# Optimization experiments

Measured on AMD Instinct MI355X. Metric: run time of the kernel, lower is better.

The kernel has to match this reference:

```python
import jax, jax.numpy as jnp
import numpy as np

N_NODES = 100_000
N_EDGES = 1_600_000
N_FEAT = 64
HIDDEN = 64
BIOPRINT = 2048
N_GRAPHS = 1024


def setup_inputs() -> dict:
    key = jax.random.key(0)
    ks = jax.random.split(key, 12)
    x = jax.random.normal(ks[0], (N_NODES, N_FEAT), jnp.float32)
    edge_index = jax.random.randint(ks[1], (2, N_EDGES), 0, N_NODES, dtype=jnp.int64)
    batch = jnp.sort(jax.random.randint(ks[2], (N_NODES,), 0, N_GRAPHS, dtype=jnp.int64))
    def lin(k, fan_in, fan_out):
        s = 1.0 / np.sqrt(fan_in)
        return jax.random.uniform(k, (fan_in, fan_out), jnp.float32, -s, s)
    W1 = lin(ks[3], N_FEAT, HIDDEN)
    b1 = jnp.zeros((HIDDEN,), jnp.float32)
    W2 = lin(ks[4], HIDDEN, HIDDEN)
    b2 = jnp.zeros((HIDDEN,), jnp.float32)
    W3 = lin(ks[5], HIDDEN, HIDDEN)
    b3 = jnp.zeros((HIDDEN,), jnp.float32)
    Wd = lin(ks[6], HIDDEN, BIOPRINT)
    bd = jax.random.uniform(ks[7], (BIOPRINT,), jnp.float32, -1.0 / np.sqrt(HIDDEN), 1.0 / np.sqrt(HIDDEN))
    return {"x": x, "edge_index": edge_index, "batch": batch,
            "W1": W1, "b1": b1, "W2": W2, "b2": b2, "W3": W3, "b3": b3,
            "Wd": Wd, "bd": bd}


def reference(x, edge_index, batch, W1, b1, W2, b2, W3, b3, Wd, bd):
    n = x.shape[0]
    src, dst = edge_index[0], edge_index[1]
    # GCN symmetric normalization with self-loops: deg = in-degree + 1
    ones_e = jnp.ones(src.shape[0], x.dtype)
    deg = jax.ops.segment_sum(ones_e, dst, num_segments=n) + 1.0
    dinv = jax.lax.rsqrt(deg)  # deg >= 1 always
    self_norm = (dinv * dinv)[:, None]
    edge_norm = (dinv[src] * dinv[dst])[:, None]

    def gcn_conv(h, W, b):
        hw = h @ W  # [N, out]
        agg = jax.ops.segment_sum(hw[src] * edge_norm, dst, num_segments=n)
        return agg + hw * self_norm + b  # self-loop handled analytically

    h = jax.nn.relu(gcn_conv(x, W1, b1))
    h = jax.nn.relu(gcn_conv(h, W2, b2))
    h = gcn_conv(h, W3, b3)

    # global_mean_pool over graph ids
    cnt = jax.ops.segment_sum(jnp.ones(n, x.dtype), batch, num_segments=N_GRAPHS)
    pooled = jax.ops.segment_sum(h, batch, num_segments=N_GRAPHS) / jnp.maximum(cnt, 1.0)[:, None]

    # dropout(p=0.5) is identity in eval mode
    logits = pooled @ Wd + bd
    probs = jax.nn.softmax(logits, axis=-1)
    return (probs >= 0.5).astype(x.dtype)
```

## Files before the change

kernel.cpp:

```cpp
#include <hip/hip_runtime.h>
#include <hip/hip_fp16.h>
#include <math.h>

#define N_NODES   100000
#define N_EDGES   1600000
#define N_FEAT    64
#define HIDDEN    64
#define BIOPRINT  2048
#define N_GRAPHS  1024

#define SENTINEL  N_NODES
#define ELL_STRIDE 64

#define N_E4 (N_EDGES / 4)
#define FILL_BLOCKS ((N_E4 + 255) / 256)
#define MM1_BLOCKS (N_NODES / 32)
#define GS_BLOCKS  5

#define XCD_SLICE 12500
#define CHUNK_SHIFT 15
#define CH4 (1 << (CHUNK_SHIFT - 2))
#define NC 49
#define SLOT_P 56
#define CNT_BLOCKS (8 * SLOT_P)
#define PREP_BLOCKS ((N_NODES + 255) / 256)

__device__ __forceinline__ __half2 shx_h2(__half2 v, int m) {
    int x = __shfl_xor(*(int*)&v, m);
    return *(__half2*)&x;
}

__device__ __forceinline__ void stage_w_perm(const float* __restrict__ W, float* sW, int t) {
    const float4* W4 = (const float4*)W;
    for (int i = t; i < 1024; i += 256) {
        float4 w = W4[i];
        int k = i >> 4;
        int c4 = (i & 15) * 4;
        int base = (k >> 2) * 256 + (k & 3);
        sW[base + (c4 + 0) * 4] = w.x;
        sW[base + (c4 + 1) * 4] = w.y;
        sW[base + (c4 + 2) * 4] = w.z;
        sW[base + (c4 + 3) * 4] = w.w;
    }
}

__global__ __launch_bounds__(256) void k_count(
        const int* __restrict__ dst, int* __restrict__ counts,
        int* __restrict__ rankl) {
    int p = blockIdx.x / SLOT_P;
    int c = blockIdx.x % SLOT_P;
    if (c >= NC) return;
    __shared__ int hist[XCD_SLICE];
    int t = threadIdx.x;
    for (int i = t; i < XCD_SLICE; i += 256) hist[i] = 0;
    __syncthreads();
    int lo = p * XCD_SLICE, hi = lo + XCD_SLICE;
    int base4 = c * CH4;
    int end4 = base4 + CH4; if (end4 > N_E4) end4 = N_E4;
    const int4* dst4 = (const int4*)dst;
    for (int i4 = base4 + t; i4 < end4; i4 += 256) {
        int4 d4 = dst4[i4];
        int e = i4 * 4;
        if (d4.x >= lo && d4.x < hi) rankl[e + 0] = atomicAdd(&hist[d4.x - lo], 1);
        if (d4.y >= lo && d4.y < hi) rankl[e + 1] = atomicAdd(&hist[d4.y - lo], 1);
        if (d4.z >= lo && d4.z < hi) rankl[e + 2] = atomicAdd(&hist[d4.z - lo], 1);
        if (d4.w >= lo && d4.w < hi) rankl[e + 3] = atomicAdd(&hist[d4.w - lo], 1);
    }
    __syncthreads();
    int* crow = counts + (size_t)c * N_NODES + lo;
    for (int i = t; i < XCD_SLICE; i += 256) crow[i] = hist[i];
}

__global__ __launch_bounds__(256) void k_prep(
        int* __restrict__ counts, int* __restrict__ deg, float* __restrict__ dinv,
        const int* __restrict__ batch, int* __restrict__ gstart) {
    int bid = blockIdx.x, t = threadIdx.x;
    if (bid < PREP_BLOCKS) {
        int n = bid * 256 + t;
        if (n >= N_NODES) return;
        int s = 0;
#pragma unroll
        for (int c = 0; c < NC; ++c) {
            size_t idx = (size_t)c * N_NODES + n;
            int v = counts[idx];
            counts[idx] = s;
            s += v;
        }
        deg[n] = s;
        dinv[n] = rsqrtf((float)s + 1.0f);
        return;
    }
    int g = (bid - PREP_BLOCKS) * 256 + t;
    if (g > N_GRAPHS) return;
    if (g == N_GRAPHS) { gstart[g] = N_NODES; return; }
    int lo = 0, hi = N_NODES;
    while (lo < hi) { int mid = (lo + hi) >> 1; if (batch[mid] < g) lo = mid + 1; else hi = mid; }
    gstart[g] = lo;
}

__global__ __launch_bounds__(256) void k_fillmm(
        const int* __restrict__ src, const int* __restrict__ dst,
        const int* __restrict__ rankl, const int* __restrict__ counts,
        int* __restrict__ colELL,
        const int* __restrict__ deg, const float* __restrict__ dinv,
        const float* __restrict__ x, const float* __restrict__ W,
        __half* __restrict__ hw) {
    int bid = blockIdx.x, t = threadIdx.x;
    if (bid < FILL_BLOCKS) {
        int tid = bid * 256 + t;
        if (tid < N_E4) {
            int e = tid * 4;
            const int* pref = counts + (size_t)(e >> CHUNK_SHIFT) * N_NODES;
            int4 d4 = ((const int4*)dst)[tid];
            int4 r4 = ((const int4*)rankl)[tid];
            int4 s4 = ((const int4*)src)[tid];
            int px = pref[d4.x] + r4.x; colELL[d4.x * ELL_STRIDE + (px & 63)] = s4.x;
            int py = pref[d4.y] + r4.y; colELL[d4.y * ELL_STRIDE + (py & 63)] = s4.y;
            int pz = pref[d4.z] + r4.z; colELL[d4.z * ELL_STRIDE + (pz & 63)] = s4.z;
            int pw = pref[d4.w] + r4.w; colELL[d4.w * ELL_STRIDE + (pw & 63)] = s4.w;
        }
        return;
    }
    bid -= FILL_BLOCKS;
    __shared__ float sW[64 * 64];
    __shared__ float sA[32 * 64];
    stage_w_perm(W, sW, t);
    int row0 = bid * 32;
    ((float4*)sA)[t]       = ((const float4*)x)[row0 * 16 + t];
    ((float4*)sA)[t + 256] = ((const float4*)x)[row0 * 16 + t + 256];
    __syncthreads();
    int wave = t >> 6, lane = t & 63;
    const float4* sWp = (const float4*)sW;
    float sum[8] = {0.f, 0.f, 0.f, 0.f, 0.f, 0.f, 0.f, 0.f};
#pragma unroll
    for (int k4 = 0; k4 < 16; ++k4) {
        float4 w4 = sWp[k4 * 64 + lane];
#pragma unroll
        for (int hh = 0; hh < 8; ++hh) {
            float4 a4 = ((const float4*)&sA[(wave * 8 + hh) * 64])[k4];
            sum[hh] = fmaf(a4.x, w4.x, sum[hh]);
            sum[hh] = fmaf(a4.y, w4.y, sum[hh]);
            sum[hh] = fmaf(a4.z, w4.z, sum[hh]);
            sum[hh] = fmaf(a4.w, w4.w, sum[hh]);
        }
    }
#pragma unroll
    for (int hh = 0; hh < 8; ++hh) {
        int row = row0 + wave * 8 + hh;
        hw[(size_t)row * 64 + lane] = __float2half_rn(sum[hh] * dinv[row]);
    }
    if (t < 32) {
        int r2 = row0 + t;
        int dv = deg[r2]; if (dv > 64) dv = 64;
        int vp = (dv + 15) & ~15;
        for (int j = dv; j < vp; ++j) colELL[r2 * ELL_STRIDE + j] = SENTINEL;
    }
}

__device__ __forceinline__ void gather2x8(
        const int* __restrict__ col, const uint4* __restrict__ hv,
        int rs, int re, int slot, int sub, float f[8]) {
    __half2 a0 = __float2half2_rn(0.f), a1 = a0, a2 = a0, a3 = a0;
    __half2 c0 = a0, c1 = a0, c2 = a0, c3 = a0;
    for (int e = rs; e < re; e += 16) {
        int s0 = __builtin_nontemporal_load(&col[e + slot]);
        int s1 = __builtin_nontemporal_load(&col[e + 2 + slot]);
        int s2 = __builtin_nontemporal_load(&col[e + 4 + slot]);
        int s3 = __builtin_nontemporal_load(&col[e + 6 + slot]);
        int s4 = __builtin_nontemporal_load(&col[e + 8 + slot]);
        int s5 = __builtin_nontemporal_load(&col[e + 10 + slot]);
        int s6 = __builtin_nontemporal_load(&col[e + 12 + slot]);
        int s7 = __builtin_nontemporal_load(&col[e + 14 + slot]);
        uint4 u0 = hv[(size_t)s0 * 8 + sub];
        uint4 u1 = hv[(size_t)s1 * 8 + sub];
        uint4 u2 = hv[(size_t)s2 * 8 + sub];
        uint4 u3 = hv[(size_t)s3 * 8 + sub];
        uint4 u4 = hv[(size_t)s4 * 8 + sub];
        uint4 u5 = hv[(size_t)s5 * 8 + sub];
        uint4 u6 = hv[(size_t)s6 * 8 + sub];
        uint4 u7 = hv[(size_t)s7 * 8 + sub];
        a0 = __hadd2(a0, *(__half2*)&u0.x); a1 = __hadd2(a1, *(__half2*)&u0.y);
        a2 = __hadd2(a2, *(__half2*)&u0.z); a3 = __hadd2(a3, *(__half2*)&u0.w);
        c0 = __hadd2(c0, *(__half2*)&u1.x); c1 = __hadd2(c1, *(__half2*)&u1.y);
        c2 = __hadd2(c2, *(__half2*)&u1.z); c3 = __hadd2(c3, *(__half2*)&u1.w);
        a0 = __hadd2(a0, *(__half2*)&u2.x); a1 = __hadd2(a1, *(__half2*)&u2.y);
        a2 = __hadd2(a2, *(__half2*)&u2.z); a3 = __hadd2(a3, *(__half2*)&u2.w);
        c0 = __hadd2(c0, *(__half2*)&u3.x); c1 = __hadd2(c1, *(__half2*)&u3.y);
        c2 = __hadd2(c2, *(__half2*)&u3.z); c3 = __hadd2(c3, *(__half2*)&u3.w);
        a0 = __hadd2(a0, *(__half2*)&u4.x); a1 = __hadd2(a1, *(__half2*)&u4.y);
        a2 = __hadd2(a2, *(__half2*)&u4.z); a3 = __hadd2(a3, *(__half2*)&u4.w);
        c0 = __hadd2(c0, *(__half2*)&u5.x); c1 = __hadd2(c1, *(__half2*)&u5.y);
        c2 = __hadd2(c2, *(__half2*)&u5.z); c3 = __hadd2(c3, *(__half2*)&u5.w);
        a0 = __hadd2(a0, *(__half2*)&u6.x); a1 = __hadd2(a1, *(__half2*)&u6.y);
        a2 = __hadd2(a2, *(__half2*)&u6.z); a3 = __hadd2(a3, *(__half2*)&u6.w);
        c0 = __hadd2(c0, *(__half2*)&u7.x); c1 = __hadd2(c1, *(__half2*)&u7.y);
        c2 = __hadd2(c2, *(__half2*)&u7.z); c3 = __hadd2(c3, *(__half2*)&u7.w);
    }
    a0 = __hadd2(a0, c0); a1 = __hadd2(a1, c1);
    a2 = __hadd2(a2, c2); a3 = __hadd2(a3, c3);
    a0 = __hadd2(a0, shx_h2(a0, 8));
    a1 = __hadd2(a1, shx_h2(a1, 8));
    a2 = __hadd2(a2, shx_h2(a2, 8));
    a3 = __hadd2(a3, shx_h2(a3, 8));
    float2 f0 = __half22float2(a0), f1 = __half22float2(a1);
    float2 f2 = __half22float2(a2), f3 = __half22float2(a3);
    f[0] = f0.x; f[1] = f0.y; f[2] = f1.x; f[3] = f1.y;
    f[4] = f2.x; f[5] = f2.y; f[6] = f3.x; f[7] = f3.y;
}

__global__ __launch_bounds__(256) void k_gmm(
        const int* __restrict__ deg, const int* __restrict__ col,
        const float* __restrict__ dinv, const float* __restrict__ b,
        const __half* __restrict__ hw_in, const float* __restrict__ W,
        __half* __restrict__ hw_out) {
    __shared__ float sW[64 * 64];
    __shared__ float sA[16 * 64];
    int t = threadIdx.x;
    stage_w_perm(W, sW, t);
    __syncthreads();

    int wave = t >> 6, lane = t & 63;
    int quarter = lane >> 4, slot = (lane >> 3) & 1, sub = lane & 7;
    int i0 = blockIdx.x * 16 + wave * 4;
    int i = i0 + quarter;
    float di = dinv[i];
    int dv = deg[i]; if (dv > 64) dv = 64;
    int rs = i * ELL_STRIDE;
    int re = rs + ((dv + 15) & ~15);
    const uint4* hv = (const uint4*)hw_in;

    float f[8];
    gather2x8(col, hv, rs, re, slot, sub, f);

    uint4 us = hv[(size_t)i * 8 + sub];
    float2 s0 = __half22float2(*(__half2*)&us.x);
    float2 s1 = __half22float2(*(__half2*)&us.y);
    float2 s2 = __half22float2(*(__half2*)&us.z);
    float2 s3 = __half22float2(*(__half2*)&us.w);
    float sf[8] = {s0.x, s0.y, s1.x, s1.y, s2.x, s2.y, s3.x, s3.y};
    float4 ba = ((const float4*)b)[sub * 2];
    float4 bb = ((const float4*)b)[sub * 2 + 1];
    float bf[8] = {ba.x, ba.y, ba.z, ba.w, bb.x, bb.y, bb.z, bb.w};
    if (slot == 0) {
        float r[8];
#pragma unroll
        for (int k = 0; k < 8; ++k) r[k] = fmaxf(fmaf(di, f[k] + sf[k], bf[k]), 0.f);
        *(float4*)&sA[(wave * 4 + quarter) * 64 + sub * 8]     = make_float4(r[0], r[1], r[2], r[3]);
        *(float4*)&sA[(wave * 4 + quarter) * 64 + sub * 8 + 4] = make_float4(r[4], r[5], r[6], r[7]);
    }

    const float4* sWp = (const float4*)sW;
    float sum[4] = {0.f, 0.f, 0.f, 0.f};
#pragma unroll
    for (int k4 = 0; k4 < 16; ++k4) {
        float4 w4 = sWp[k4 * 64 + lane];
#pragma unroll
        for (int hh = 0; hh < 4; ++hh) {
            float4 a4 = ((const float4*)&sA[(wave * 4 + hh) * 64])[k4];
            sum[hh] = fmaf(a4.x, w4.x, sum[hh]);
            sum[hh] = fmaf(a4.y, w4.y, sum[hh]);
            sum[hh] = fmaf(a4.z, w4.z, sum[hh]);
            sum[hh] = fmaf(a4.w, w4.w, sum[hh]);
        }
    }
#pragma unroll
    for (int hh = 0; hh < 4; ++hh)
        hw_out[(size_t)(i0 + hh) * 64 + lane] = __float2half_rn(sum[hh] * dinv[i0 + hh]);
}

__global__ __launch_bounds__(256) void k_gather3(
        const int* __restrict__ deg, const int* __restrict__ col,
        const float* __restrict__ dinv, const float* __restrict__ b,
        const __half* __restrict__ hw_in, __half* __restrict__ conv) {
    int t = threadIdx.x;
    int wave = t >> 6, lane = t & 63;
    int quarter = lane >> 4, slot = (lane >> 3) & 1, sub = lane & 7;
    int i = blockIdx.x * 16 + wave * 4 + quarter;
    float di = dinv[i];
    int dv = deg[i]; if (dv > 64) dv = 64;
    int rs = i * ELL_STRIDE;
    int re = rs + ((dv + 15) & ~15);
    const uint4* hv = (const uint4*)hw_in;

    float f[8];
    gather2x8(col, hv, rs, re, slot, sub, f);

    if (slot == 0) {
        uint4 us = hv[(size_t)i * 8 + sub];
        float2 s0 = __half22float2(*(__half2*)&us.x);
        float2 s1 = __half22float2(*(__half2*)&us.y);
        float2 s2 = __half22float2(*(__half2*)&us.z);
        float2 s3 = __half22float2(*(__half2*)&us.w);
        float sf[8] = {s0.x, s0.y, s1.x, s1.y, s2.x, s2.y, s3.x, s3.y};
        float4 ba = ((const float4*)b)[sub * 2];
        float4 bb = ((const float4*)b)[sub * 2 + 1];
        float bf[8] = {ba.x, ba.y, ba.z, ba.w, bb.x, bb.y, bb.z, bb.w};
        uint4 o;
        __half2* oh = (__half2*)&o;
#pragma unroll
        for (int c = 0; c < 4; ++c) {
            float r0 = fmaf(di, f[2 * c] + sf[2 * c], bf[2 * c]);
            float r1 = fmaf(di, f[2 * c + 1] + sf[2 * c + 1], bf[2 * c + 1]);
            oh[c] = __halves2half2(__float2half_rn(r0), __float2half_rn(r1));
        }
        ((uint4*)conv)[(size_t)i * 8 + sub] = o;
    }
}

__global__ __launch_bounds__(256) void k_dense(
        const __half* __restrict__ conv, const int* __restrict__ gstart,
        const float* __restrict__ Wd, const float* __restrict__ bd,
        float* __restrict__ out) {
    __shared__ float sred[4][64];
    __shared__ float sp[64];
    __shared__ float rmax[4];
    __shared__ float rsum[4];
    int t = threadIdx.x;
    int wave = t >> 6, lane = t & 63;
    int g = blockIdx.x;
    int n0 = gstart[g], n1 = gstart[g + 1];

    int fp = lane & 31;
    int par = lane >> 5;
    const __half2* conv2 = (const __half2*)conv;
    float2 acc2 = make_float2(0.f, 0.f);
    for (int i = n0 + wave * 2 + par; i < n1; i += 8) {
        float2 f = __half22float2(conv2[(size_t)i * 32 + fp]);
        acc2.x += f.x; acc2.y += f.y;
    }
    acc2.x += __shfl_xor(acc2.x, 32);
    acc2.y += __shfl_xor(acc2.y, 32);
    if (lane < 32) { sred[wave][2 * fp] = acc2.x; sred[wave][2 * fp + 1] = acc2.y; }
    __syncthreads();
    if (t < 64) {
        int n = n1 - n0;
        float s = sred[0][t] + sred[1][t] + sred[2][t] + sred[3][t];
        sp[t] = (n > 0) ? s / (float)n : 0.f;
    }
    __syncthreads();

    float acc[8];
#pragma unroll
    for (int r = 0; r < 8; ++r) acc[r] = bd[r * 256 + t];
    for (int k = 0; k < 64; ++k) {
        float h = sp[k];
#pragma unroll
        for (int r = 0; r < 8; ++r)
            acc[r] = fmaf(h, Wd[k * BIOPRINT + r * 256 + t], acc[r]);
    }

    float m = acc[0];
#pragma unroll
    for (int r = 1; r < 8; ++r) m = fmaxf(m, acc[r]);
#pragma unroll
    for (int off = 32; off > 0; off >>= 1) m = fmaxf(m, __shfl_xor(m, off));
    if (lane == 0) rmax[wave] = m;
    __syncthreads();
    m = fmaxf(fmaxf(rmax[0], rmax[1]), fmaxf(rmax[2], rmax[3]));

    float s = 0.f;
#pragma unroll
    for (int r = 0; r < 8; ++r) { acc[r] = expf(acc[r] - m); s += acc[r]; }
#pragma unroll
    for (int off = 32; off > 0; off >>= 1) s += __shfl_xor(s, off);
    if (lane == 0) rsum[wave] = s;
    __syncthreads();
    s = rsum[0] + rsum[1] + rsum[2] + rsum[3];

#pragma unroll
    for (int r = 0; r < 8; ++r) {
        float p = acc[r] / s;
        out[(size_t)g * BIOPRINT + r * 256 + t] = (p >= 0.5f) ? 1.0f : 0.0f;
    }
}


extern "C" void kernel_launch(void* const* d_in, const int* in_sizes, int n_in,
                              void* d_out, int out_size, void* d_ws, size_t ws_size,
                              hipStream_t stream) {
    const float* x     = (const float*)d_in[0];
    const int*   ei    = (const int*)d_in[1];
    const int*   batch = (const int*)d_in[2];
    const float* W1 = (const float*)d_in[3];
    const float* b1 = (const float*)d_in[4];
    const float* W2 = (const float*)d_in[5];
    const float* b2 = (const float*)d_in[6];
    const float* W3 = (const float*)d_in[7];
    const float* b3 = (const float*)d_in[8];
    const float* Wd = (const float*)d_in[9];
    const float* bd = (const float*)d_in[10];
    float* out = (float*)d_out;

    const int* src = ei;
    const int* dst = ei + N_EDGES;

    char* ws = (char*)d_ws;
    size_t off = 0;
    auto alloc = [&](size_t bytes) {
        void* p = ws + off;
        off += (bytes + 255) & ~(size_t)255;
        return p;
    };
    int*    deg    = (int*)alloc(N_NODES * sizeof(int));
    float*  dinv   = (float*)alloc(N_NODES * sizeof(float));
    int*    rank   = (int*)alloc((size_t)N_EDGES * sizeof(int));
    int*    gstart = (int*)alloc((N_GRAPHS + 1) * sizeof(int));
    int*    counts = (int*)alloc((size_t)NC * N_NODES * sizeof(int));
    int*    colELL = (int*)alloc((size_t)N_NODES * ELL_STRIDE * sizeof(int));
    __half* bufA   = (__half*)alloc((size_t)(N_NODES + 1) * HIDDEN * sizeof(__half));
    __half* bufB   = (__half*)alloc((size_t)(N_NODES + 1) * HIDDEN * sizeof(__half));
    __half* conv   = (__half*)alloc((size_t)N_NODES * HIDDEN * sizeof(__half));

    hipMemsetAsync(bufA + (size_t)N_NODES * HIDDEN, 0, HIDDEN * sizeof(__half), stream);
    hipMemsetAsync(bufB + (size_t)N_NODES * HIDDEN, 0, HIDDEN * sizeof(__half), stream);

    k_count<<<CNT_BLOCKS, 256, 0, stream>>>(dst, counts, rank);
    k_prep<<<PREP_BLOCKS + GS_BLOCKS, 256, 0, stream>>>(counts, deg, dinv, batch, gstart);
    k_fillmm<<<FILL_BLOCKS + MM1_BLOCKS, 256, 0, stream>>>(
        src, dst, rank, counts, colELL, deg, dinv, x, W1, bufA);

    const int g16_grid = N_NODES / 16;
    k_gmm<<<g16_grid, 256, 0, stream>>>(deg, colELL, dinv, b1, bufA, W2, bufB);
    k_gmm<<<g16_grid, 256, 0, stream>>>(deg, colELL, dinv, b2, bufB, W3, bufA);
    k_gather3<<<g16_grid, 256, 0, stream>>>(deg, colELL, dinv, b3, bufA, conv);
    k_dense<<<N_GRAPHS, 256, 0, stream>>>(conv, gstart, Wd, bd, out);
}
```

Before: 316.4 us.

## Shrink count/rank arrays and move first matmul into count kernel

The per-chunk prefix counts are stored as 16-bit and the per-edge local ranks as 8-bit, which cuts the traffic of the count, prep and fill stages. The layer-1 x@W1 matmul moves into the count kernel, where it runs alongside the histogram blocks. The dinv scaling is now applied in a separate in-place pass inside the fill kernel. In exchange the fill kernel does an extra read-modify-write of bufA, and the 8-bit ranks assume per-chunk, per-node counts stay below 256.

Measured after the change: 309.2 us. 2.3% less time.

```diff
diff --git a/kernel.cpp b/kernel.cpp
--- a/kernel.cpp
+++ b/kernel.cpp
@@ -24,6 +24,9 @@
 #define SLOT_P 56
 #define CNT_BLOCKS (8 * SLOT_P)
 #define PREP_BLOCKS ((N_NODES + 255) / 256)
+
+typedef unsigned short u16;
+typedef unsigned char  u8;
 
 __device__ __forceinline__ __half2 shx_h2(__half2 v, int m) {
     int x = __shfl_xor(*(int*)&v, m);
@@ -44,35 +47,68 @@
     }
 }
 
-__global__ __launch_bounds__(256) void k_count(
-        const int* __restrict__ dst, int* __restrict__ counts,
-        int* __restrict__ rankl) {
-    int p = blockIdx.x / SLOT_P;
-    int c = blockIdx.x % SLOT_P;
-    if (c >= NC) return;
-    __shared__ int hist[XCD_SLICE];
-    int t = threadIdx.x;
-    for (int i = t; i < XCD_SLICE; i += 256) hist[i] = 0;
-    __syncthreads();
-    int lo = p * XCD_SLICE, hi = lo + XCD_SLICE;
-    int base4 = c * CH4;
-    int end4 = base4 + CH4; if (end4 > N_E4) end4 = N_E4;
-    const int4* dst4 = (const int4*)dst;
-    for (int i4 = base4 + t; i4 < end4; i4 += 256) {
-        int4 d4 = dst4[i4];
-        int e = i4 * 4;
-        if (d4.x >= lo && d4.x < hi) rankl[e + 0] = atomicAdd(&hist[d4.x - lo], 1);
-        if (d4.y >= lo && d4.y < hi) rankl[e + 1] = atomicAdd(&hist[d4.y - lo], 1);
-        if (d4.z >= lo && d4.z < hi) rankl[e + 2] = atomicAdd(&hist[d4.z - lo], 1);
-        if (d4.w >= lo && d4.w < hi) rankl[e + 3] = atomicAdd(&hist[d4.w - lo], 1);
-    }
-    __syncthreads();
-    int* crow = counts + (size_t)c * N_NODES + lo;
-    for (int i = t; i < XCD_SLICE; i += 256) crow[i] = hist[i];
+__global__ __launch_bounds__(256) void k_countmm(
+        const int* __restrict__ dst, u16* __restrict__ counts, u8* __restrict__ rankl,
+        const float* __restrict__ x, const float* __restrict__ W,
+        __half* __restrict__ hw) {
+    __shared__ int smem[XCD_SLICE];
+    int bid = blockIdx.x, t = threadIdx.x;
+    if (bid < CNT_BLOCKS) {
+        int p = bid / SLOT_P;
+        int c = bid % SLOT_P;
+        if (c >= NC) return;
+        int* hist = smem;
+        for (int i = t; i < XCD_SLICE; i += 256) hist[i] = 0;
+        __syncthreads();
+        int lo = p * XCD_SLICE, hi = lo + XCD_SLICE;
+        int base4 = c * CH4;
+        int end4 = base4 + CH4; if (end4 > N_E4) end4 = N_E4;
+        const int4* dst4 = (const int4*)dst;
+        for (int i4 = base4 + t; i4 < end4; i4 += 256) {
+            int4 d4 = dst4[i4];
+            int e = i4 * 4;
+            if (d4.x >= lo && d4.x < hi) rankl[e + 0] = (u8)atomicAdd(&hist[d4.x - lo], 1);
+            if (d4.y >= lo && d4.y < hi) rankl[e + 1] = (u8)atomicAdd(&hist[d4.y - lo], 1);
+            if (d4.z >= lo && d4.z < hi) rankl[e + 2] = (u8)atomicAdd(&hist[d4.z - lo], 1);
+            if (d4.w >= lo && d4.w < hi) rankl[e + 3] = (u8)atomicAdd(&hist[d4.w - lo], 1);
+        }
+        __syncthreads();
+        u16* crow = counts + (size_t)c * N_NODES + lo;
+        for (int i = t; i < XCD_SLICE; i += 256) crow[i] = (u16)hist[i];
+        return;
+    }
+    bid -= CNT_BLOCKS;
+    float* sW = (float*)smem;
+    float* sA = (float*)smem + 4096;
+    stage_w_perm(W, sW, t);
+    int row0 = bid * 32;
+    ((float4*)sA)[t]       = ((const float4*)x)[row0 * 16 + t];
+    ((float4*)sA)[t + 256] = ((const float4*)x)[row0 * 16 + t + 256];
+    __syncthreads();
+    int wave = t >> 6, lane = t & 63;
+    const float4* sWp = (const float4*)sW;
+    float sum[8] = {0.f, 0.f, 0.f, 0.f, 0.f, 0.f, 0.f, 0.f};
+#pragma unroll
+    for (int k4 = 0; k4 < 16; ++k4) {
+        float4 w4 = sWp[k4 * 64 + lane];
+#pragma unroll
+        for (int hh = 0; hh < 8; ++hh) {
+            float4 a4 = ((const float4*)&sA[(wave * 8 + hh) * 64])[k4];
+            sum[hh] = fmaf(a4.x, w4.x, sum[hh]);
+            sum[hh] = fmaf(a4.y, w4.y, sum[hh]);
+            sum[hh] = fmaf(a4.z, w4.z, sum[hh]);
+            sum[hh] = fmaf(a4.w, w4.w, sum[hh]);
+        }
+    }
+#pragma unroll
+    for (int hh = 0; hh < 8; ++hh) {
+        int row = row0 + wave * 8 + hh;
+        hw[(size_t)row * 64 + lane] = __float2half_rn(sum[hh]);
+    }
 }
 
 __global__ __launch_bounds__(256) void k_prep(
-        int* __restrict__ counts, int* __restrict__ deg, float* __restrict__ dinv,
+        u16* __restrict__ counts, int* __restrict__ deg, float* __restrict__ dinv,
         const int* __restrict__ batch, int* __restrict__ gstart) {
     int bid = blockIdx.x, t = threadIdx.x;
     if (bid < PREP_BLOCKS) {
@@ -83,7 +119,7 @@
         for (int c = 0; c < NC; ++c) {
             size_t idx = (size_t)c * N_NODES + n;
             int v = counts[idx];
-            counts[idx] = s;
+            counts[idx] = (u16)s;
             s += v;
         }
         deg[n] = s;
@@ -98,21 +134,20 @@
     gstart[g] = lo;
 }
 
-__global__ __launch_bounds__(256) void k_fillmm(
+__global__ __launch_bounds__(256) void k_fillscale(
         const int* __restrict__ src, const int* __restrict__ dst,
-        const int* __restrict__ rankl, const int* __restrict__ counts,
+        const u8* __restrict__ rankl, const u16* __restrict__ counts,
         int* __restrict__ colELL,
         const int* __restrict__ deg, const float* __restrict__ dinv,
-        const float* __restrict__ x, const float* __restrict__ W,
         __half* __restrict__ hw) {
     int bid = blockIdx.x, t = threadIdx.x;
     if (bid < FILL_BLOCKS) {
         int tid = bid * 256 + t;
         if (tid < N_E4) {
             int e = tid * 4;
-            const int* pref = counts + (size_t)(e >> CHUNK_SHIFT) * N_NODES;
+            const u16* pref = counts + (size_t)(e >> CHUNK_SHIFT) * N_NODES;
             int4 d4 = ((const int4*)dst)[tid];
-            int4 r4 = ((const int4*)rankl)[tid];
+            uchar4 r4 = ((const uchar4*)rankl)[tid];
             int4 s4 = ((const int4*)src)[tid];
             int px = pref[d4.x] + r4.x; colELL[d4.x * ELL_STRIDE + (px & 63)] = s4.x;
             int py = pref[d4.y] + r4.y; colELL[d4.y * ELL_STRIDE + (py & 63)] = s4.y;
@@ -122,33 +157,18 @@
         return;
     }
     bid -= FILL_BLOCKS;
-    __shared__ float sW[64 * 64];
-    __shared__ float sA[32 * 64];
-    stage_w_perm(W, sW, t);
     int row0 = bid * 32;
-    ((float4*)sA)[t]       = ((const float4*)x)[row0 * 16 + t];
-    ((float4*)sA)[t + 256] = ((const float4*)x)[row0 * 16 + t + 256];
-    __syncthreads();
-    int wave = t >> 6, lane = t & 63;
-    const float4* sWp = (const float4*)sW;
-    float sum[8] = {0.f, 0.f, 0.f, 0.f, 0.f, 0.f, 0.f, 0.f};
-#pragma unroll
-    for (int k4 = 0; k4 < 16; ++k4) {
-        float4 w4 = sWp[k4 * 64 + lane];
-#pragma unroll
-        for (int hh = 0; hh < 8; ++hh) {
-            float4 a4 = ((const float4*)&sA[(wave * 8 + hh) * 64])[k4];
-            sum[hh] = fmaf(a4.x, w4.x, sum[hh]);
-            sum[hh] = fmaf(a4.y, w4.y, sum[hh]);
-            sum[hh] = fmaf(a4.z, w4.z, sum[hh]);
-            sum[hh] = fmaf(a4.w, w4.w, sum[hh]);
-        }
-    }
-#pragma unroll
-    for (int hh = 0; hh < 8; ++hh) {
-        int row = row0 + wave * 8 + hh;
-        hw[(size_t)row * 64 + lane] = __float2half_rn(sum[hh] * dinv[row]);
-    }
+    int row = row0 + (t >> 3);
+    float di = dinv[row];
+    uint4* p = (uint4*)hw;
+    uint4 v = p[(size_t)row * 8 + (t & 7)];
+    __half2* h2 = (__half2*)&v;
+#pragma unroll
+    for (int c = 0; c < 4; ++c) {
+        float2 f = __half22float2(h2[c]);
+        h2[c] = __halves2half2(__float2half_rn(f.x * di), __float2half_rn(f.y * di));
+    }
+    p[(size_t)row * 8 + (t & 7)] = v;
     if (t < 32) {
         int r2 = row0 + t;
         int dv = deg[r2]; if (dv > 64) dv = 64;
@@ -403,9 +423,9 @@
     };
     int*    deg    = (int*)alloc(N_NODES * sizeof(int));
     float*  dinv   = (float*)alloc(N_NODES * sizeof(float));
-    int*    rank   = (int*)alloc((size_t)N_EDGES * sizeof(int));
+    u8*     rankl  = (u8*)alloc((size_t)N_EDGES * sizeof(u8));
     int*    gstart = (int*)alloc((N_GRAPHS + 1) * sizeof(int));
-    int*    counts = (int*)alloc((size_t)NC * N_NODES * sizeof(int));
+    u16*    counts = (u16*)alloc((size_t)NC * N_NODES * sizeof(u16));
     int*    colELL = (int*)alloc((size_t)N_NODES * ELL_STRIDE * sizeof(int));
     __half* bufA   = (__half*)alloc((size_t)(N_NODES + 1) * HIDDEN * sizeof(__half));
     __half* bufB   = (__half*)alloc((size_t)(N_NODES + 1) * HIDDEN * sizeof(__half));
@@ -414,10 +434,10 @@
     hipMemsetAsync(bufA + (size_t)N_NODES * HIDDEN, 0, HIDDEN * sizeof(__half), stream);
     hipMemsetAsync(bufB + (size_t)N_NODES * HIDDEN, 0, HIDDEN * sizeof(__half), stream);
 
-    k_count<<<CNT_BLOCKS, 256, 0, stream>>>(dst, counts, rank);
+    k_countmm<<<CNT_BLOCKS + MM1_BLOCKS, 256, 0, stream>>>(dst, counts, rankl, x, W1, bufA);
     k_prep<<<PREP_BLOCKS + GS_BLOCKS, 256, 0, stream>>>(counts, deg, dinv, batch, gstart);
-    k_fillmm<<<FILL_BLOCKS + MM1_BLOCKS, 256, 0, stream>>>(
-        src, dst, rank, counts, colELL, deg, dinv, x, W1, bufA);
+    k_fillscale<<<FILL_BLOCKS + MM1_BLOCKS, 256, 0, stream>>>(
+        src, dst, rankl, counts, colELL, deg, dinv, bufA);
 
     const int g16_grid = N_NODES / 16;
     k_gmm<<<g16_grid, 256, 0, stream>>>(deg, colELL, dinv, b1, bufA, W2, bufB);
```
